# Performance work log

Hardware: AMD Instinct MI355X
Metric: run time of the kernel (lower is better)

## Reference

```python
import jax, jax.numpy as jnp
import numpy as np

B, E, S, W, M, C, O = 2048, 16, 512, 512, 64, 64, 8

def hardsigmoid(x):
    return jnp.clip((x + 3.0) / 6.0, 0.0, 1.0)

def swish(x):
    return x * jax.nn.sigmoid(x)

def setup_inputs() -> dict:
    key = jax.random.key(0)
    ks = jax.random.split(key, 16)
    scale = 1.0  # 1/(in_channels*out_channels) with in=out=1
    d = {}
    d["x"] = jax.random.normal(ks[0], (B, E * S), jnp.float32)
    d["codes"] = jax.random.normal(ks[1], (E, C), jnp.float32) * 0.1
    d["p_w"] = jax.random.normal(ks[2], (2 * W, 2 * S), jnp.float32) * 0.02
    d["p_b"] = jnp.zeros((2 * W,), jnp.float32)
    d["com0"] = jax.random.uniform(ks[3], (M, 2), jnp.float32) * scale
    d["code0"] = jax.random.uniform(ks[4], (C, M, 2), jnp.float32) * scale
    d["filt0"] = -3.0 * jnp.ones((M,), jnp.float32)
    d["com1"] = jax.random.uniform(ks[5], (M, 2), jnp.float32) * scale
    d["code1"] = jax.random.uniform(ks[6], (C, M, 2), jnp.float32) * scale
    d["filt1"] = -3.0 * jnp.ones((M,), jnp.float32)
    d["w0_w"] = jax.random.normal(ks[7], (2 * W, 2 * W), jnp.float32) * 0.02
    d["w0_b"] = jnp.zeros((2 * W,), jnp.float32)
    d["w1_w"] = jax.random.normal(ks[8], (2 * W, 2 * W), jnp.float32) * 0.02
    d["w1_b"] = jnp.zeros((2 * W,), jnp.float32)
    # fc1: Conv1d(2W -> (O//2)*W, k=1, groups=W): per group 2 in -> O//2 out
    d["fc1_w"] = jax.random.normal(ks[9], (W, O // 2, 2), jnp.float32) * 0.1
    d["fc1_b"] = jnp.zeros((W * (O // 2),), jnp.float32)
    d["fc2_w"] = jax.random.normal(ks[10], (O, W * (O // 2)), jnp.float32) * 0.02
    d["fc2_b"] = jnp.zeros((O,), jnp.float32)
    return d

def spectral(x3, codes, com, codew, filt):
    # x3: [B, E, L] with in_channels=out_channels=1; L = 2*W
    L = x3.shape[-1]
    m = filt.shape[0]
    xf = jnp.fft.rfft(x3, axis=-1)                      # [B, E, L//2+1] complex64
    lam = hardsigmoid(filt)                              # [m]
    com_c = com[:, 0] + 1j * com[:, 1]                   # [m]
    env = jnp.einsum('ec,cmk->emk', codes, codew)        # [E, m, 2]
    env_c = env[..., 0] + 1j * env[..., 1]               # [E, m]
    xm = xf[:, :, :m]                                    # [B, E, m]
    out_m = lam * xm * com_c + (1.0 - lam) * xm * env_c[None]
    out_f = jnp.zeros_like(xf).at[:, :, :m].set(out_m)
    return jnp.fft.irfft(out_f, n=L, axis=-1)            # [B, E, L]

def reference(x, codes, p_w, p_b, com0, code0, filt0, com1, code1, filt1,
              w0_w, w0_b, w1_w, w1_b, fc1_w, fc1_b, fc2_w, fc2_b):
    bsz = x.shape[0]
    e = codes.shape[0]
    s = x.shape[1] // e
    xv = x.reshape(bsz, e, s)
    grid = jnp.broadcast_to(jnp.linspace(0.0, 1.0, s, dtype=x.dtype), (bsz, e, s))
    h = jnp.concatenate([xv, grid], axis=-1).reshape(bsz * e, 2 * s)
    h = h @ p_w.T + p_b                                  # [BE, 2W]
    twoW = h.shape[-1]
    h3 = h.reshape(bsz, e, twoW)
    x1 = spectral(h3, codes, com0, code0, filt0)
    x2 = h @ w0_w.T + w0_b
    h3 = swish(x1 + x2.reshape(bsz, e, twoW))
    h = h3.reshape(bsz * e, twoW)
    x1 = spectral(h3, codes, com1, code1, filt1)
    x2 = h @ w1_w.T + w1_b
    h = (x1 + x2.reshape(bsz, e, twoW)).reshape(bsz * e, twoW)
    # grouped pointwise fc1: groups = W, 2 in-ch per group -> O//2 out-ch per group
    wd = fc1_w.shape[0]
    hg = h.reshape(bsz * e, wd, 2)
    h = jnp.einsum('ngk,gok->ngo', hg, fc1_w).reshape(bsz * e, -1) + fc1_b
    h = swish(h)
    h = h @ fc2_w.T + fc2_b                              # [BE, O]
    return h.reshape(bsz, -1)                            # [B, E*O]
```

## Files before the change

kernel.cpp:

```cpp
#include <hip/hip_runtime.h>
#include <hip/hip_bf16.h>
#include <cstdint>


typedef __bf16 bf16;
typedef __attribute__((ext_vector_type(8))) __bf16 bf16x8;
typedef __attribute__((ext_vector_type(4))) __bf16 bf16x4;
typedef __attribute__((ext_vector_type(4))) float f32x4;

#define N_ROWS 32768

__device__ __forceinline__ void gl_lds16(const void* g, void* l) {
    __builtin_amdgcn_global_load_lds(
        (const __attribute__((address_space(1))) void*)g,
        (__attribute__((address_space(3))) void*)l,
        16, 0, 0);
}

__device__ __forceinline__ float swishf(float v) {
    return v / (1.f + __expf(-v));
}


__global__ __launch_bounds__(256) void build_cmix(const float* __restrict__ codes,
                                                  const float* __restrict__ com,
                                                  const float* __restrict__ code,
                                                  const float* __restrict__ filt,
                                                  float2* __restrict__ cmix) {
    int t = blockIdx.x * 256 + threadIdx.x;
    if (t >= 16 * 64) return;
    int e = t >> 6, m = t & 63;
    float er = 0.f, ei = 0.f;
    for (int c = 0; c < 64; ++c) {
        float cd = codes[e * 64 + c];
        er += cd * code[(c * 64 + m) * 2 + 0];
        ei += cd * code[(c * 64 + m) * 2 + 1];
    }
    float f = filt[m];
    float lam = fminf(fmaxf((f + 3.f) * (1.f / 6.f), 0.f), 1.f);
    float cr = lam * com[m * 2 + 0] + (1.f - lam) * er;
    float ci = lam * com[m * 2 + 1] + (1.f - lam) * ei;
    float g = (m == 0) ? (1.f / 1024.f) : (2.f / 1024.f);
    cmix[t] = make_float2(g * cr, g * ci);
}

__global__ __launch_bounds__(256) void build_fb(bf16* __restrict__ Fb) {
    int t = blockIdx.x * 256 + threadIdx.x;
    int rr = t >> 10, s = t & 1023;
    int k = rr >> 1;
    int ph = (k * s) & 1023;
    float ang = (float)ph * 6.1359231515425649e-3f;
    float v = (rr & 1) ? -sinf(ang) : cosf(ang);
    Fb[t] = (bf16)v;
}

__global__ __launch_bounds__(256) void build_bcat(const float* __restrict__ w,
                                                  bf16* __restrict__ out) {
    int t = blockIdx.x * 256 + threadIdx.x;
    if (t >= 1024 * 1152) return;
    int j = t / 1152, c = t % 1152;
    float v;
    if (c < 1024) {
        v = w[j * 1024 + c];
    } else {
        int cc = c - 1024, k = cc >> 1;
        int ph = (k * j) & 1023;
        float ang = (float)ph * 6.1359231515425649e-3f;
        v = (cc & 1) ? -sinf(ang) : cosf(ang);
    }
    out[t] = (bf16)v;
}

__global__ __launch_bounds__(256) void convert_bf16(const float* __restrict__ in,
                                                    bf16* __restrict__ out, int n) {
    int t = blockIdx.x * 256 + threadIdx.x;
    if (t < n) out[t] = (bf16)in[t];
}

__global__ __launch_bounds__(256) void build_a0(const float* __restrict__ x,
                                                bf16* __restrict__ A0) {
    int t = blockIdx.x * 256 + threadIdx.x;
    int n = t >> 7, part = t & 127;
    bf16x8 o;
    if (part < 64) {
        const float4* xp = (const float4*)(x + ((size_t)n * 512 + part * 8));
        float4 a = xp[0], b = xp[1];
        o[0] = (bf16)a.x; o[1] = (bf16)a.y; o[2] = (bf16)a.z; o[3] = (bf16)a.w;
        o[4] = (bf16)b.x; o[5] = (bf16)b.y; o[6] = (bf16)b.z; o[7] = (bf16)b.w;
        *(bf16x8*)(A0 + (size_t)n * 1024 + part * 8) = o;
    } else {
        int s0 = (part - 64) * 8;
        #pragma unroll
        for (int j = 0; j < 8; ++j) o[j] = (bf16)((float)(s0 + j) * (1.0f / 511.0f));
        *(bf16x8*)(A0 + (size_t)n * 1024 + 512 + s0) = o;
    }
}

template<int ACT>
__global__ __launch_bounds__(512, 2)
void gemm256(const bf16* __restrict__ A, int lda,
             const bf16* __restrict__ Bt, int ldb,
             const float* __restrict__ bias,
             bf16* __restrict__ Cout, int ldc,
             int K) {
    __shared__ bf16 sA[2][256 * 64];
    __shared__ bf16 sB[2][256 * 64];
    const int tid = threadIdx.x;
    const int wave = tid >> 6, lane = tid & 63;
    const int wm = wave >> 2, wn = wave & 3;
    const int rowA0 = blockIdx.x * 256;
    const int rowB0 = blockIdx.y * 256;

    f32x4 acc[8][4];
    #pragma unroll
    for (int m = 0; m < 8; ++m)
        #pragma unroll
        for (int n = 0; n < 4; ++n)
            acc[m][n] = f32x4{0.f, 0.f, 0.f, 0.f};

    const int srq = lane >> 3;
    const int ssl = (lane & 7) ^ srq;
    const bf16* gA = A + (size_t)(rowA0 + wave * 8 + srq) * lda + ssl * 8;
    const bf16* gB = Bt + (size_t)(rowB0 + wave * 8 + srq) * ldb + ssl * 8;

    const int NT = K / 64;
    auto STAGE = [&](int t) {
        const int slot = t & 1;
        const size_t ko = (size_t)t * 64;
        #pragma unroll
        for (int j = 0; j < 4; ++j) {
            gl_lds16(gA + (size_t)j * 64 * lda + ko, &sA[slot][(j * 64 + wave * 8) * 64]);
            gl_lds16(gB + (size_t)j * 64 * ldb + ko, &sB[slot][(j * 64 + wave * 8) * 64]);
        }
    };

    STAGE(0);

    const int p = lane & 15, q = lane >> 4;
    const int axr = (p & 7) << 4;

    for (int t = 0; t < NT; ++t) {
        asm volatile("s_waitcnt vmcnt(0)" ::: "memory");
        __builtin_amdgcn_s_barrier();
        __builtin_amdgcn_sched_barrier(0);
        if (t + 1 < NT) STAGE(t + 1);
        const char* sa = (const char*)sA[t & 1];
        const char* sb = (const char*)sB[t & 1];
        #pragma unroll
        for (int kk = 0; kk < 64; kk += 32) {
            bf16x8 af[8], bfr[4];
            #pragma unroll
            for (int m = 0; m < 8; ++m) {
                int off = (((wm * 128 + m * 16 + p) * 64 + kk + q * 8) * 2) ^ axr;
                af[m] = *(const bf16x8*)(sa + off);
            }
            #pragma unroll
            for (int n = 0; n < 4; ++n) {
                int off = (((wn * 64 + n * 16 + p) * 64 + kk + q * 8) * 2) ^ axr;
                bfr[n] = *(const bf16x8*)(sb + off);
            }
            asm volatile("s_waitcnt lgkmcnt(0)" ::: "memory");
            __builtin_amdgcn_sched_barrier(0);
            __builtin_amdgcn_s_setprio(1);
            #pragma unroll
            for (int m = 0; m < 8; ++m)
                #pragma unroll
                for (int n = 0; n < 4; ++n)
                    acc[m][n] = __builtin_amdgcn_mfma_f32_16x16x32_bf16(af[m], bfr[n], acc[m][n], 0, 0, 0);
            __builtin_amdgcn_s_setprio(0);
            __builtin_amdgcn_sched_barrier(0);
        }
    }

    const int rowb = rowA0 + wm * 128;
    const int colb = rowB0 + wn * 64;
    #pragma unroll
    for (int m = 0; m < 8; ++m) {
        #pragma unroll
        for (int n = 0; n < 4; ++n) {
            int col = colb + n * 16 + p;
            float bv = bias ? bias[col] : 0.f;
            #pragma unroll
            for (int r = 0; r < 4; ++r) {
                int row = rowb + m * 16 + q * 4 + r;
                float v = acc[m][n][r] + bv;
                if (ACT) v = swishf(v);
                Cout[(size_t)row * ldc + col] = (bf16)v;
            }
        }
    }
}

__global__ __launch_bounds__(256)
void gemm_mix(const bf16* __restrict__ A, int lda,
              const bf16* __restrict__ Bt, int ldb,
              void* __restrict__ Cout, int ldc,
              const float2* __restrict__ cmix,
              int K) {
    __shared__ bf16 sA[128 * 64];
    __shared__ bf16 sB[128 * 64];
    const int tid = threadIdx.x;
    const int wave = tid >> 6;
    const int lane = tid & 63;
    const int wm = wave >> 1, wn = wave & 1;
    const int rowA0 = blockIdx.x * 128;

    f32x4 acc[4][4];
    #pragma unroll
    for (int m = 0; m < 4; ++m)
        #pragma unroll
        for (int n = 0; n < 4; ++n)
            acc[m][n] = f32x4{0.f, 0.f, 0.f, 0.f};

    const int srow = wave * 32 + (lane >> 3);
    const int scol = (lane & 7) * 8;
    const bf16* gA = A + (size_t)(rowA0 + srow) * lda + scol;
    const bf16* gB = Bt + (size_t)srow * ldb + scol;
    bf16* lA = &sA[(wave * 32) * 64];
    bf16* lB = &sB[(wave * 32) * 64];

    for (int k0 = 0; k0 < K; k0 += 64) {
        __syncthreads();
        #pragma unroll
        for (int i = 0; i < 4; ++i) {
            gl_lds16(gA + (size_t)i * 8 * lda + k0, lA + i * 8 * 64);
            gl_lds16(gB + (size_t)i * 8 * ldb + k0, lB + i * 8 * 64);
        }
        __syncthreads();
        #pragma unroll
        for (int kk = 0; kk < 64; kk += 32) {
            bf16x8 af[4], bfr[4];
            #pragma unroll
            for (int m = 0; m < 4; ++m)
                af[m] = *(const bf16x8*)&sA[(wm * 64 + m * 16 + (lane & 15)) * 64 + kk + ((lane >> 4) * 8)];
            #pragma unroll
            for (int n = 0; n < 4; ++n)
                bfr[n] = *(const bf16x8*)&sB[(wn * 64 + n * 16 + (lane & 15)) * 64 + kk + ((lane >> 4) * 8)];
            #pragma unroll
            for (int m = 0; m < 4; ++m)
                #pragma unroll
                for (int n = 0; n < 4; ++n)
                    acc[m][n] = __builtin_amdgcn_mfma_f32_16x16x32_bf16(af[m], bfr[n], acc[m][n], 0, 0, 0);
        }
    }

    const int rowb = rowA0 + wm * 64;
    #pragma unroll
    for (int m = 0; m < 4; ++m) {
        #pragma unroll
        for (int n = 0; n < 4; ++n) {
            int col = wn * 64 + n * 16 + (lane & 15);
            int k = col >> 1;
            #pragma unroll
            for (int r = 0; r < 4; ++r) {
                float v = acc[m][n][r];
                float pp = __shfl_xor(v, 1);
                int row = rowb + m * 16 + (lane >> 4) * 4 + r;
                float2 c = cmix[(row & 15) * 64 + k];
                float val = v * c.x + (((lane & 1) == 0) ? -pp * c.y : pp * c.y);
                ((bf16*)Cout)[(size_t)row * ldc + col] = (bf16)val;
            }
        }
    }
}

__global__ __launch_bounds__(256) void fc_fused(const bf16* __restrict__ H,
                                                const float* __restrict__ w1,
                                                const float* __restrict__ b1,
                                                const float* __restrict__ w2,
                                                const float* __restrict__ b2,
                                                float* __restrict__ out) {
    __shared__ bf16 sw2[8][2048];
    __shared__ bf16 ss[2048];
    int tid = threadIdx.x;
    for (int i = tid * 4; i < 8 * 2048; i += 1024) {
        float4 v = *(const float4*)(w2 + i);
        bf16x4 b = {(bf16)v.x, (bf16)v.y, (bf16)v.z, (bf16)v.w};
        *(bf16x4*)&sw2[0][i] = b;
    }

    float wv[16];
    const float4* w1p = (const float4*)(w1 + tid * 16);
    *(float4*)&wv[0]  = w1p[0];
    *(float4*)&wv[4]  = w1p[1];
    *(float4*)&wv[8]  = w1p[2];
    *(float4*)&wv[12] = w1p[3];
    float bb[8];
    const float4* b1p = (const float4*)(b1 + tid * 8);
    *(float4*)&bb[0] = b1p[0];
    *(float4*)&bb[4] = b1p[1];
    __syncthreads();

    for (int r = 0; r < 16; ++r) {
        int n = blockIdx.x * 16 + r;
        bf16x4 hv = *(const bf16x4*)(H + (size_t)n * 1024 + tid * 4);
        float hh[4] = {(float)hv[0], (float)hv[1], (float)hv[2], (float)hv[3]};
        bf16x8 sb;
        #pragma unroll
        for (int jj = 0; jj < 8; ++jj) {
            float h0 = hh[(jj >> 2) * 2];
            float h1 = hh[(jj >> 2) * 2 + 1];
            float t = h0 * wv[2 * jj] + h1 * wv[2 * jj + 1] + bb[jj];
            sb[jj] = (bf16)swishf(t);
        }
        *(bf16x8*)&ss[tid * 8] = sb;
        __syncthreads();
        int o8 = tid >> 5, l5 = tid & 31;
        float p = 0.f;
        #pragma unroll
        for (int i = 0; i < 16; ++i) {
            bf16x4 a = *(const bf16x4*)&ss[4 * l5 + 128 * i];
            bf16x4 b = *(const bf16x4*)&sw2[o8][4 * l5 + 128 * i];
            p += (float)a[0] * (float)b[0] + (float)a[1] * (float)b[1]
               + (float)a[2] * (float)b[2] + (float)a[3] * (float)b[3];
        }
        #pragma unroll
        for (int msk = 1; msk < 32; msk <<= 1) p += __shfl_xor(p, msk);
        if (l5 == 0) out[(size_t)n * 8 + o8] = p + b2[o8];
        __syncthreads();
    }
}


extern "C" void kernel_launch(void* const* d_in, const int* in_sizes, int n_in,
                              void* d_out, int out_size, void* d_ws, size_t ws_size,
                              hipStream_t stream) {
    const float* x     = (const float*)d_in[0];
    const float* codes = (const float*)d_in[1];
    const float* p_w   = (const float*)d_in[2];
    const float* p_b   = (const float*)d_in[3];
    const float* com0  = (const float*)d_in[4];
    const float* code0 = (const float*)d_in[5];
    const float* filt0 = (const float*)d_in[6];
    const float* com1  = (const float*)d_in[7];
    const float* code1 = (const float*)d_in[8];
    const float* filt1 = (const float*)d_in[9];
    const float* w0_w  = (const float*)d_in[10];
    const float* w0_b  = (const float*)d_in[11];
    const float* w1_w  = (const float*)d_in[12];
    const float* w1_b  = (const float*)d_in[13];
    const float* fc1w  = (const float*)d_in[14];
    const float* fc1b  = (const float*)d_in[15];
    const float* fc2w  = (const float*)d_in[16];
    const float* fc2b  = (const float*)d_in[17];
    float* out = (float*)d_out;

    char* ws = (char*)d_ws;
    bf16*  pwb  = (bf16*)(ws + 0);
    bf16*  B0   = (bf16*)(ws + 2097152);
    bf16*  B1   = (bf16*)(ws + 4456448);
    bf16*  Fb   = (bf16*)(ws + 6815744);
    float2* cm0 = (float2*)(ws + 7077888);
    float2* cm1 = (float2*)(ws + 7086080);
    const size_t CB = 7094272;

    const size_t PER_ROW = 2048 + 2304 + 2304;
    long rmax = 0;
    if (ws_size > CB) rmax = (long)((ws_size - CB) / PER_ROW) / 256 * 256;
    if (rmax > N_ROWS) rmax = N_ROWS;
    if (rmax < 256) {
        hipMemsetAsync(d_out, 0, (size_t)out_size * sizeof(float), stream);
        return;
    }
    const int R = (int)rmax;

    build_cmix<<<4, 256, 0, stream>>>(codes, com0, code0, filt0, cm0);
    build_cmix<<<4, 256, 0, stream>>>(codes, com1, code1, filt1, cm1);
    build_fb<<<512, 256, 0, stream>>>(Fb);
    build_bcat<<<4608, 256, 0, stream>>>(w0_w, B0);
    build_bcat<<<4608, 256, 0, stream>>>(w1_w, B1);
    convert_bf16<<<4096, 256, 0, stream>>>(p_w, pwb, 1024 * 1024);

    char* cb = ws + CB;
    for (int row0 = 0; row0 < N_ROWS; row0 += R) {
        const int r = (N_ROWS - row0 < R) ? (N_ROWS - row0) : R;
        bf16*  A0  = (bf16*)cb;
        bf16*  H3b = (bf16*)cb;
        bf16*  A1  = (bf16*)(cb + (size_t)R * 2048);
        bf16*  A2  = (bf16*)(cb + (size_t)R * 2048 + (size_t)R * 2304);

        build_a0<<<r / 2, 256, 0, stream>>>(x + (size_t)row0 * 512, A0);

        gemm256<0><<<dim3(r / 256, 4), 512, 0, stream>>>(
            A0, 1024, pwb, 1024, p_b, A1, 1152, 1024);
        gemm_mix<<<dim3(r / 128, 1), 256, 0, stream>>>(
            A1, 1152, Fb, 1024, (void*)(A1 + 1024), 1152, cm0, 1024);
        gemm256<1><<<dim3(r / 256, 4), 512, 0, stream>>>(
            A1, 1152, B0, 1152, w0_b, A2, 1152, 1152);
        gemm_mix<<<dim3(r / 128, 1), 256, 0, stream>>>(
            A2, 1152, Fb, 1024, (void*)(A2 + 1024), 1152, cm1, 1024);
        gemm256<0><<<dim3(r / 256, 4), 512, 0, stream>>>(
            A2, 1152, B1, 1152, w1_b, H3b, 1024, 1152);
        fc_fused<<<r / 16, 256, 0, stream>>>(H3b, fc1w, fc1b, fc2w, fc2b, out + (size_t)row0 * 8);
    }
}
```

Measured before the change: 467.6 us.

## Fold constant grid and first DFT into precomputed projection weights

The constant linspace grid half of the input projection is folded into a precomputed bias, so the first GEMM uses K=512 instead of 1024. The first spectral DFT is composed with the projection weights (G = F·p_w) and appended as extra output columns, with the complex mode mix applied in the GEMM epilogue via lane shuffles. This removes one gemm_mix launch and halves the first GEMM's reduction depth. In exchange it adds setup kernels that compute the composed weights in fp32, and it changes rounding because the DFT is applied before bf16 quantization rather than after.

Result: slower. 608.9 us (+30.2%).

```diff
diff --git a/kernel.cpp b/kernel.cpp
--- a/kernel.cpp
+++ b/kernel.cpp
@@ -44,14 +44,16 @@
     cmix[t] = make_float2(g * cr, g * ci);
 }
 
-__global__ __launch_bounds__(256) void build_fb(bf16* __restrict__ Fb) {
+__global__ __launch_bounds__(256) void build_fb2(float* __restrict__ Fb32,
+                                                 bf16* __restrict__ Fbb) {
     int t = blockIdx.x * 256 + threadIdx.x;
     int rr = t >> 10, s = t & 1023;
     int k = rr >> 1;
     int ph = (k * s) & 1023;
     float ang = (float)ph * 6.1359231515425649e-3f;
     float v = (rr & 1) ? -sinf(ang) : cosf(ang);
-    Fb[t] = (bf16)v;
+    Fb32[t] = v;
+    Fbb[t] = (bf16)v;
 }
 
 __global__ __launch_bounds__(256) void build_bcat(const float* __restrict__ w,
@@ -71,37 +73,75 @@
     out[t] = (bf16)v;
 }
 
-__global__ __launch_bounds__(256) void convert_bf16(const float* __restrict__ in,
-                                                    bf16* __restrict__ out, int n) {
+__global__ __launch_bounds__(256) void build_g(const float* __restrict__ Fb32,
+                                               const float* __restrict__ p_w,
+                                               float* __restrict__ G32) {
+    int c = blockIdx.x * 256 + threadIdx.x;
+    int k0 = blockIdx.y * 4;
+    float a0 = 0.f, a1 = 0.f, a2 = 0.f, a3 = 0.f;
+    #pragma unroll 4
+    for (int w = 0; w < 1024; ++w) {
+        float pv = p_w[(size_t)w * 1024 + c];
+        a0 += Fb32[(k0 + 0) * 1024 + w] * pv;
+        a1 += Fb32[(k0 + 1) * 1024 + w] * pv;
+        a2 += Fb32[(k0 + 2) * 1024 + w] * pv;
+        a3 += Fb32[(k0 + 3) * 1024 + w] * pv;
+    }
+    G32[(k0 + 0) * 512 + c] = a0;
+    G32[(k0 + 1) * 512 + c] = a1;
+    G32[(k0 + 2) * 512 + c] = a2;
+    G32[(k0 + 3) * 512 + c] = a3;
+}
+
+__global__ __launch_bounds__(256) void build_bias1a(const float* __restrict__ p_w,
+                                                    const float* __restrict__ p_b,
+                                                    float* __restrict__ bias1) {
+    int w = blockIdx.x * 256 + threadIdx.x;
+    if (w >= 1024) return;
+    float s = 0.f;
+    for (int i = 0; i < 512; ++i)
+        s += ((float)i * (1.f / 511.f)) * p_w[(size_t)w * 1024 + 512 + i];
+    bias1[w] = p_b[w] + s;
+}
+
+__global__ __launch_bounds__(128) void build_bias1b(const float* __restrict__ Fb32,
+                                                    float* __restrict__ bias1) {
+    int k2 = threadIdx.x;
+    float s = 0.f;
+    for (int w = 0; w < 1024; ++w) s += Fb32[k2 * 1024 + w] * bias1[w];
+    bias1[1024 + k2] = s;
+    bias1[1152 + k2] = 0.f;
+}
+
+__global__ __launch_bounds__(256) void build_wp(const float* __restrict__ p_w,
+                                                const float* __restrict__ G32,
+                                                bf16* __restrict__ WP) {
     int t = blockIdx.x * 256 + threadIdx.x;
-    if (t < n) out[t] = (bf16)in[t];
-}
-
-__global__ __launch_bounds__(256) void build_a0(const float* __restrict__ x,
-                                                bf16* __restrict__ A0) {
+    if (t >= 1280 * 512) return;
+    int r = t >> 9, c = t & 511;
+    float v = (r < 1024) ? p_w[(size_t)r * 1024 + c]
+            : (r < 1152) ? G32[(r - 1024) * 512 + c] : 0.f;
+    WP[t] = (bf16)v;
+}
+
+__global__ __launch_bounds__(256) void convert_x(const float* __restrict__ x,
+                                                 bf16* __restrict__ A0) {
     int t = blockIdx.x * 256 + threadIdx.x;
-    int n = t >> 7, part = t & 127;
+    const float4* xp = (const float4*)(x + (size_t)t * 8);
+    float4 a = xp[0], b = xp[1];
     bf16x8 o;
-    if (part < 64) {
-        const float4* xp = (const float4*)(x + ((size_t)n * 512 + part * 8));
-        float4 a = xp[0], b = xp[1];
-        o[0] = (bf16)a.x; o[1] = (bf16)a.y; o[2] = (bf16)a.z; o[3] = (bf16)a.w;
-        o[4] = (bf16)b.x; o[5] = (bf16)b.y; o[6] = (bf16)b.z; o[7] = (bf16)b.w;
-        *(bf16x8*)(A0 + (size_t)n * 1024 + part * 8) = o;
-    } else {
-        int s0 = (part - 64) * 8;
-        #pragma unroll
-        for (int j = 0; j < 8; ++j) o[j] = (bf16)((float)(s0 + j) * (1.0f / 511.0f));
-        *(bf16x8*)(A0 + (size_t)n * 1024 + 512 + s0) = o;
-    }
-}
-
-template<int ACT>
+    o[0] = (bf16)a.x; o[1] = (bf16)a.y; o[2] = (bf16)a.z; o[3] = (bf16)a.w;
+    o[4] = (bf16)b.x; o[5] = (bf16)b.y; o[6] = (bf16)b.z; o[7] = (bf16)b.w;
+    *(bf16x8*)(A0 + (size_t)t * 8) = o;
+}
+
+template<int ACT, int HASMIX>
 __global__ __launch_bounds__(512, 2)
 void gemm256(const bf16* __restrict__ A, int lda,
              const bf16* __restrict__ Bt, int ldb,
              const float* __restrict__ bias,
              bf16* __restrict__ Cout, int ldc,
+             const float2* __restrict__ cmix, int ncols,
              int K) {
     __shared__ bf16 sA[2][256 * 64];
     __shared__ bf16 sB[2][256 * 64];
@@ -184,8 +224,18 @@
             for (int r = 0; r < 4; ++r) {
                 int row = rowb + m * 16 + q * 4 + r;
                 float v = acc[m][n][r] + bv;
-                if (ACT) v = swishf(v);
-                Cout[(size_t)row * ldc + col] = (bf16)v;
+                if (HASMIX) {
+                    float pp = __shfl_xor(v, 1);
+                    if (col >= 1024) {
+                        int k = (col - 1024) >> 1;
+                        float2 c = cmix[(row & 15) * 64 + k];
+                        v = v * c.x + (((p & 1) == 0) ? -pp * c.y : pp * c.y);
+                    }
+                    if (col < ncols) Cout[(size_t)row * ldc + col] = (bf16)v;
+                } else {
+                    if (ACT) v = swishf(v);
+                    Cout[(size_t)row * ldc + col] = (bf16)v;
+                }
             }
         }
     }
@@ -346,13 +396,16 @@
     float* out = (float*)d_out;
 
     char* ws = (char*)d_ws;
-    bf16*  pwb  = (bf16*)(ws + 0);
-    bf16*  B0   = (bf16*)(ws + 2097152);
-    bf16*  B1   = (bf16*)(ws + 4456448);
-    bf16*  Fb   = (bf16*)(ws + 6815744);
-    float2* cm0 = (float2*)(ws + 7077888);
-    float2* cm1 = (float2*)(ws + 7086080);
-    const size_t CB = 7094272;
+    bf16*  WP   = (bf16*)(ws + 0);
+    bf16*  B0   = (bf16*)(ws + 1310720);
+    bf16*  B1   = (bf16*)(ws + 3670016);
+    bf16*  Fbb  = (bf16*)(ws + 6029312);
+    float* Fb32 = (float*)(ws + 6291456);
+    float* G32  = (float*)(ws + 6815744);
+    float* bias1= (float*)(ws + 7077888);
+    float2* cm0 = (float2*)(ws + 7083008);
+    float2* cm1 = (float2*)(ws + 7091200);
+    const size_t CB = 7099392;
 
     const size_t PER_ROW = 2048 + 2304 + 2304;
     long rmax = 0;
@@ -366,10 +419,13 @@
 
     build_cmix<<<4, 256, 0, stream>>>(codes, com0, code0, filt0, cm0);
     build_cmix<<<4, 256, 0, stream>>>(codes, com1, code1, filt1, cm1);
-    build_fb<<<512, 256, 0, stream>>>(Fb);
+    build_fb2<<<512, 256, 0, stream>>>(Fb32, Fbb);
     build_bcat<<<4608, 256, 0, stream>>>(w0_w, B0);
     build_bcat<<<4608, 256, 0, stream>>>(w1_w, B1);
-    convert_bf16<<<4096, 256, 0, stream>>>(p_w, pwb, 1024 * 1024);
+    build_g<<<dim3(2, 32), 256, 0, stream>>>(Fb32, p_w, G32);
+    build_bias1a<<<4, 256, 0, stream>>>(p_w, p_b, bias1);
+    build_bias1b<<<1, 128, 0, stream>>>(Fb32, bias1);
+    build_wp<<<2560, 256, 0, stream>>>(p_w, G32, WP);
 
     char* cb = ws + CB;
     for (int row0 = 0; row0 < N_ROWS; row0 += R) {
@@ -379,18 +435,16 @@
         bf16*  A1  = (bf16*)(cb + (size_t)R * 2048);
         bf16*  A2  = (bf16*)(cb + (size_t)R * 2048 + (size_t)R * 2304);
 
-        build_a0<<<r / 2, 256, 0, stream>>>(x + (size_t)row0 * 512, A0);
-
-        gemm256<0><<<dim3(r / 256, 4), 512, 0, stream>>>(
-            A0, 1024, pwb, 1024, p_b, A1, 1152, 1024);
+        convert_x<<<r / 4, 256, 0, stream>>>(x + (size_t)row0 * 512, A0);
+
+        gemm256<0, 1><<<dim3(r / 256, 5), 512, 0, stream>>>(
+            A0, 512, WP, 512, bias1, A1, 1152, cm0, 1152, 512);
+        gemm256<1, 0><<<dim3(r / 256, 4), 512, 0, stream>>>(
+            A1, 1152, B0, 1152, w0_b, A2, 1152, nullptr, 1024, 1152);
         gemm_mix<<<dim3(r / 128, 1), 256, 0, stream>>>(
-            A1, 1152, Fb, 1024, (void*)(A1 + 1024), 1152, cm0, 1024);
-        gemm256<1><<<dim3(r / 256, 4), 512, 0, stream>>>(
-            A1, 1152, B0, 1152, w0_b, A2, 1152, 1152);
-        gemm_mix<<<dim3(r / 128, 1), 256, 0, stream>>>(
-            A2, 1152, Fb, 1024, (void*)(A2 + 1024), 1152, cm1, 1024);
-        gemm256<0><<<dim3(r / 256, 4), 512, 0, stream>>>(
-            A2, 1152, B1, 1152, w1_b, H3b, 1024, 1152);
+            A2, 1152, Fbb, 1024, (void*)(A2 + 1024), 1152, cm1, 1024);
+        gemm256<0, 0><<<dim3(r / 256, 4), 512, 0, stream>>>(
+            A2, 1152, B1, 1152, w1_b, H3b, 1024, nullptr, 1024, 1152);
         fc_fused<<<r / 16, 256, 0, stream>>>(H3b, fc1w, fc1b, fc2w, fc2b, out + (size_t)row0 * 8);
     }
 }
```
